# Performance work log

Hardware: AMD Instinct MI355X
Metric: run time of the kernel (lower is better)

## Reference

```python
import jax, jax.numpy as jnp
import numpy as np

B, N, DIM = 2, 2048, 1024
HEADS, DIM_HEAD = 16, 64
SCALE = DIM_HEAD ** -0.5
MASK_VALUE = -jnp.finfo(jnp.float32).max


def setup_inputs() -> dict:
    key = jax.random.key(0)
    ks = jax.random.split(key, 7)
    inner = HEADS * DIM_HEAD
    x = jax.random.normal(ks[0], (B, N, DIM), dtype=jnp.float32)
    mask = jax.random.randint(ks[1], (B, 1, N, N), 0, 2, dtype=jnp.int32)
    Wq = jax.random.normal(ks[2], (DIM, inner), dtype=jnp.float32) * (DIM ** -0.5)
    Wk = jax.random.normal(ks[3], (DIM, inner), dtype=jnp.float32) * (DIM ** -0.5)
    Wv = jax.random.normal(ks[4], (DIM, inner), dtype=jnp.float32) * (DIM ** -0.5)
    Wo = jax.random.normal(ks[5], (inner, DIM), dtype=jnp.float32) * (inner ** -0.5)
    bo = jnp.zeros((DIM,), dtype=jnp.float32)
    return {"x": x, "mask": mask, "Wq": Wq, "Wk": Wk, "Wv": Wv, "Wo": Wo, "bo": bo}


def reference(x, mask, Wq, Wk, Wv, Wo, bo):
    b, n, _ = x.shape
    # projections -> [b, h, n, d]
    def split_heads(t):
        return t.reshape(b, n, HEADS, DIM_HEAD).transpose(0, 2, 1, 3)
    q = split_heads(x @ Wq)
    k = split_heads(x @ Wk)
    v = split_heads(x @ Wv)
    # full attention scores [b, h, i, j]
    dots = jnp.einsum('bhid,bhjd->bhij', q, k) * SCALE
    # faithful to source: bin_mask = (mask == 0); fill where ~bin_mask
    bin_mask = (mask == 0)
    dots = jnp.where(bin_mask, dots, MASK_VALUE)
    attn = jax.nn.softmax(dots, axis=-1)  # dropout p=0.0 -> identity
    out = jnp.einsum('bhij,bhjd->bhid', attn, v)
    out = out.transpose(0, 2, 1, 3).reshape(b, n, HEADS * DIM_HEAD)
    return out @ Wo + bo
```

## Files before the change

### kernel.cpp

```cpp
#include <hip/hip_runtime.h>
#include <cstdint>
#include <cstddef>

typedef float    f32x4  __attribute__((ext_vector_type(4)));
typedef __bf16   bf16x8 __attribute__((ext_vector_type(8)));
typedef unsigned u32x4  __attribute__((ext_vector_type(4)));
typedef unsigned u32x2  __attribute__((ext_vector_type(2)));
typedef unsigned short u16;
typedef unsigned int   u32;

#define SCL2E 0.18033688011112042f

static __device__ __forceinline__ u16 f2bf(float f) {
    u32 u = __builtin_bit_cast(u32, f);
    u32 r = (u + 0x7FFFu + ((u >> 16) & 1u)) >> 16;
    return (u16)r;
}

static __device__ __forceinline__ u32 cvtpk_bf16(float lo, float hi) {
    u32 r;
    asm("v_cvt_pk_bf16_f32 %0, %1, %2" : "=v"(r) : "v"(lo), "v"(hi));
    return r;
}

static __device__ __forceinline__ float fexp2(float x) {
    float r;
    asm("v_exp_f32 %0, %1" : "=v"(r) : "v"(x));
    return r;
}

static __device__ __forceinline__ void gll16(const u16* g, void* l) {
    __builtin_amdgcn_global_load_lds((const __attribute__((address_space(1))) void*)g,
                                     (__attribute__((address_space(3))) void*)l, 16, 0, 0);
}


__global__ __launch_bounds__(256) void prep_k(
    const float* __restrict__ x, u16* __restrict__ xb,
    const float* __restrict__ W0, const float* __restrict__ W1,
    const float* __restrict__ W2, const float* __restrict__ W3,
    u16* __restrict__ T0, u16* __restrict__ T1,
    u16* __restrict__ T2, u16* __restrict__ T3,
    const int* __restrict__ mask, u32* __restrict__ mp)
{
    __shared__ float T[64][65];
    const int bid = blockIdx.x;
    if (bid < 2048) {
        const long i = ((long)bid * 256 + threadIdx.x) * 8;
        f32x4 a = *(const f32x4*)(x + i);
        f32x4 c = *(const f32x4*)(x + i + 4);
        u32x4 o;
        o[0] = (u32)f2bf(a[0]) | ((u32)f2bf(a[1]) << 16);
        o[1] = (u32)f2bf(a[2]) | ((u32)f2bf(a[3]) << 16);
        o[2] = (u32)f2bf(c[0]) | ((u32)f2bf(c[1]) << 16);
        o[3] = (u32)f2bf(c[2]) | ((u32)f2bf(c[3]) << 16);
        *(u32x4*)(xb + i) = o;
    } else if (bid < 3072) {
        const int idx = bid - 2048;
        const int z = idx >> 8, rem = idx & 255;
        const int n0 = (rem & 15) * 64, k0 = (rem >> 4) * 64;
        const float* W = (z == 0) ? W0 : (z == 1) ? W1 : (z == 2) ? W2 : W3;
        u16* Wt = (z == 0) ? T0 : (z == 1) ? T1 : (z == 2) ? T2 : T3;
        const float scl = (z == 0) ? SCL2E : 1.0f;
        const int c = threadIdx.x & 63, r0 = (threadIdx.x >> 6) * 16;
#pragma unroll
        for (int i = 0; i < 16; ++i)
            T[r0 + i][c] = W[(long)(k0 + r0 + i) * 1024 + n0 + c];
        __syncthreads();
#pragma unroll
        for (int i = 0; i < 16; ++i)
            Wt[(long)(n0 + r0 + i) * 1024 + k0 + c] = f2bf(T[c][r0 + i] * scl);
    } else {
        const long wi = (long)(bid - 3072) * 256 + threadIdx.x;
        const int* src = mask + wi * 32;
        u32 word = 0;
#pragma unroll
        for (int c = 0; c < 8; ++c) {
            const int4 v = *(const int4*)(src + c * 4);
            word |= (u32)(v.x != 0) << (c * 4);
            word |= (u32)(v.y != 0) << (c * 4 + 1);
            word |= (u32)(v.z != 0) << (c * 4 + 2);
            word |= (u32)(v.w != 0) << (c * 4 + 3);
        }
        mp[wi] = word;
    }
}

__global__ __launch_bounds__(256) void vt_k(const u16* __restrict__ v, u16* __restrict__ vt) {
    __shared__ u16 T[64][66];
    const int nt = blockIdx.x, h = blockIdx.y, b = blockIdx.z;
    const int c = threadIdx.x & 63, r0 = (threadIdx.x >> 6) * 16;
    const u16* src = v + ((long)b * 2048 + nt * 64) * 1024 + h * 64;
    u16* dst = vt + ((long)(b * 16 + h) * 64) * 2048 + nt * 64;
#pragma unroll
    for (int i = 0; i < 16; ++i)
        T[r0 + i][c] = src[(long)(r0 + i) * 1024 + c];
    __syncthreads();
#pragma unroll
    for (int i = 0; i < 16; ++i)
        dst[(long)(r0 + i) * 2048 + c] = T[c][r0 + i];
}


__global__ __launch_bounds__(256, 3) void gemm_qkv(
    const u16* __restrict__ A, const u16* __restrict__ Bt, u16* __restrict__ C0)
{
    constexpr int K = 1024;
    __shared__ u16 As[2][128 * 32];
    __shared__ u16 Bs[2][128 * 32];
    const int tid = threadIdx.x;
    const int wave = tid >> 6, lane = tid & 63;
    const int wr = wave >> 1, wc = wave & 1;
    const int g = lane >> 4, lr = lane & 15;
    const long mBase = (long)blockIdx.y * 128;
    const long nBase = (long)blockIdx.x * 128;

    f32x4 acc[4][4];
#pragma unroll
    for (int i = 0; i < 4; ++i)
#pragma unroll
        for (int j = 0; j < 4; ++j) acc[i][j] = f32x4{0.f, 0.f, 0.f, 0.f};

    const int o0 = tid * 16, o1 = (256 + tid) * 16;
    const int r0 = o0 >> 6, cb0 = o0 & 63;
    const int r1 = o1 >> 6, cb1 = o1 & 63;

    gll16(A  + (mBase + r0) * K + (cb0 >> 1), (char*)&As[0][0] + o0);
    gll16(A  + (mBase + r1) * K + (cb1 >> 1), (char*)&As[0][0] + o1);
    gll16(Bt + (nBase + r0) * K + (cb0 >> 1), (char*)&Bs[0][0] + o0);
    gll16(Bt + (nBase + r1) * K + (cb1 >> 1), (char*)&Bs[0][0] + o1);
    __syncthreads();

#pragma unroll 2
    for (int kt = 0; kt < 32; ++kt) {
        const int buf = kt & 1;
        if (kt + 1 < 32) {
            const long ko = (long)(kt + 1) * 32;
            gll16(A  + (mBase + r0) * K + ko + (cb0 >> 1), (char*)&As[buf ^ 1][0] + o0);
            gll16(A  + (mBase + r1) * K + ko + (cb1 >> 1), (char*)&As[buf ^ 1][0] + o1);
            gll16(Bt + (nBase + r0) * K + ko + (cb0 >> 1), (char*)&Bs[buf ^ 1][0] + o0);
            gll16(Bt + (nBase + r1) * K + ko + (cb1 >> 1), (char*)&Bs[buf ^ 1][0] + o1);
        }
        bf16x8 af[4], bfv[4];
#pragma unroll
        for (int mi = 0; mi < 4; ++mi)
            af[mi] = *(const bf16x8*)((const char*)&As[buf][0] + (wr * 64 + mi * 16 + lr) * 64 + g * 16);
#pragma unroll
        for (int ni = 0; ni < 4; ++ni)
            bfv[ni] = *(const bf16x8*)((const char*)&Bs[buf][0] + (wc * 64 + ni * 16 + lr) * 64 + g * 16);
#pragma unroll
        for (int mi = 0; mi < 4; ++mi)
#pragma unroll
            for (int ni = 0; ni < 4; ++ni)
                acc[mi][ni] = __builtin_amdgcn_mfma_f32_16x16x32_bf16(af[mi], bfv[ni], acc[mi][ni], 0, 0, 0);
        __syncthreads();
    }

    const int wsel = (int)(nBase >> 10);
    u16* Cw = C0 + (long)wsel * (4096l * 1024);
    const long ncl = nBase & 1023;
#pragma unroll
    for (int mi = 0; mi < 4; ++mi)
#pragma unroll
        for (int r = 0; r < 4; ++r) {
            const long row = mBase + wr * 64 + mi * 16 + g * 4 + r;
#pragma unroll
            for (int ni = 0; ni < 4; ++ni) {
                const long col = ncl + wc * 64 + ni * 16 + lr;
                Cw[row * 1024 + col] = f2bf(acc[mi][ni][r]);
            }
        }
}


__global__ __launch_bounds__(256, 2) void gemm_out(
    const u16* __restrict__ A, const u16* __restrict__ Bt,
    float* __restrict__ Cf, const float* __restrict__ bias)
{
    constexpr int K = 1024, N = 1024;
    __shared__ u16 As[2][64 * 32];
    __shared__ u16 Bs[2][128 * 32];
    const int tid = threadIdx.x;
    const int wave = tid >> 6, lane = tid & 63;
    const int wr = wave >> 1, wc = wave & 1;
    const int g = lane >> 4, lr = lane & 15;
    const long mBase = (long)blockIdx.y * 64;
    const long nBase = (long)blockIdx.x * 128;

    f32x4 acc[2][4];
#pragma unroll
    for (int i = 0; i < 2; ++i)
#pragma unroll
        for (int j = 0; j < 4; ++j) acc[i][j] = f32x4{0.f, 0.f, 0.f, 0.f};

    const int oA = tid * 16;
    const int rA = oA >> 6, cbA = oA & 63;
    const int o0 = tid * 16, o1 = (256 + tid) * 16;
    const int r0 = o0 >> 6, cb0 = o0 & 63;
    const int r1 = o1 >> 6, cb1 = o1 & 63;

    gll16(A  + (mBase + rA) * K + (cbA >> 1), (char*)&As[0][0] + oA);
    gll16(Bt + (nBase + r0) * K + (cb0 >> 1), (char*)&Bs[0][0] + o0);
    gll16(Bt + (nBase + r1) * K + (cb1 >> 1), (char*)&Bs[0][0] + o1);
    __syncthreads();

#pragma unroll 2
    for (int kt = 0; kt < 32; ++kt) {
        const int buf = kt & 1;
        if (kt + 1 < 32) {
            const long ko = (long)(kt + 1) * 32;
            gll16(A  + (mBase + rA) * K + ko + (cbA >> 1), (char*)&As[buf ^ 1][0] + oA);
            gll16(Bt + (nBase + r0) * K + ko + (cb0 >> 1), (char*)&Bs[buf ^ 1][0] + o0);
            gll16(Bt + (nBase + r1) * K + ko + (cb1 >> 1), (char*)&Bs[buf ^ 1][0] + o1);
        }
        bf16x8 af[2], bfv[4];
#pragma unroll
        for (int mi = 0; mi < 2; ++mi)
            af[mi] = *(const bf16x8*)((const char*)&As[buf][0] + (wr * 32 + mi * 16 + lr) * 64 + g * 16);
#pragma unroll
        for (int ni = 0; ni < 4; ++ni)
            bfv[ni] = *(const bf16x8*)((const char*)&Bs[buf][0] + (wc * 64 + ni * 16 + lr) * 64 + g * 16);
#pragma unroll
        for (int mi = 0; mi < 2; ++mi)
#pragma unroll
            for (int ni = 0; ni < 4; ++ni)
                acc[mi][ni] = __builtin_amdgcn_mfma_f32_16x16x32_bf16(af[mi], bfv[ni], acc[mi][ni], 0, 0, 0);
        __syncthreads();
    }

#pragma unroll
    for (int mi = 0; mi < 2; ++mi)
#pragma unroll
        for (int r = 0; r < 4; ++r) {
            const long row = mBase + wr * 32 + mi * 16 + g * 4 + r;
#pragma unroll
            for (int ni = 0; ni < 4; ++ni) {
                const long col = nBase + wc * 64 + ni * 16 + lr;
                Cf[row * N + col] = acc[mi][ni][r] + bias[col];
            }
        }
}


__global__ __launch_bounds__(512, 2) void attn_fwd(
    const u16* __restrict__ Qg_, const u16* __restrict__ Kg_, const u16* __restrict__ Vtg_,
    const u32* __restrict__ maskp, u16* __restrict__ Og_)
{
    __shared__ u16 Ks[2][2][64 * 64];
    __shared__ u16 Vs[2][2][64 * 64];

    const int tid = threadIdx.x, w = tid >> 6, lane = tid & 63;
    const int g = lane >> 4, lr = lane & 15;
    const int L = blockIdx.x;
    const int slot = L >> 3;
    const int grp = (L & 7) + 8 * (slot >> 3);
    const int q0 = (slot & 7) * 256;
    const int b = grp >> 4, h = grp & 15;
    const u16* Qg = Qg_ + ((long)b * 2048) * 1024 + h * 64;
    const u16* Kg = Kg_ + ((long)b * 2048) * 1024 + h * 64;
    const u16* Vtg = Vtg_ + ((long)grp * 64) * 2048;
    u16* Og = Og_ + ((long)b * 2048) * 1024 + h * 64;

    const int ldso = tid * 16;
    const int m = ldso >> 7, cb = ldso & 127;
    const int sb = cb ^ ((m & 7) << 4);
    const int kap = ((m >> 4) & 1) * 32 + ((m >> 2) & 3) * 8 + ((m >> 5) & 1) * 4 + (m & 3);
    const long ksrc = (long)kap * 1024 + (sb >> 1);
    const long vsrc = (long)m * 2048 + (sb >> 1);

    bf16x8 qf[2][2];
#pragma unroll
    for (int nq = 0; nq < 2; ++nq)
#pragma unroll
        for (int ks = 0; ks < 2; ++ks)
            qf[nq][ks] = *(const bf16x8*)(Qg + (long)(q0 + w * 32 + nq * 16 + lr) * 1024 + ks * 32 + g * 8);

    const long mrow0 = (long)b * 2048 + q0 + w * 32 + lr;
    const u32* mpr0 = maskp + mrow0 * 64;
    const u32* mpr1 = maskp + (mrow0 + 16) * 64;

    u32x4 mwC0 = *(const u32x4*)(mpr0);
    u32x4 mwC1 = *(const u32x4*)(mpr1);
#pragma unroll
    for (int hh = 0; hh < 2; ++hh) {
        gll16(Kg + hh * 65536 + ksrc, (char*)&Ks[0][hh][0] + ldso);
        gll16(Vtg + hh * 64 + vsrc, (char*)&Vs[0][hh][0] + ldso);
    }
    __syncthreads();

    const int swz = (lr & 7) << 4;
    int kb[2];
#pragma unroll
    for (int ks = 0; ks < 2; ++ks) kb[ks] = (ks * 64 + g * 16) ^ swz;

    f32x4 oacc[2][4];
#pragma unroll
    for (int i = 0; i < 2; ++i)
#pragma unroll
        for (int j = 0; j < 4; ++j) oacc[i][j] = f32x4{0.f, 0.f, 0.f, 0.f};
    f32x4 osum[2];
    osum[0] = f32x4{0.f, 0.f, 0.f, 0.f};
    osum[1] = f32x4{0.f, 0.f, 0.f, 0.f};
    const f32x4 z4 = {0.f, 0.f, 0.f, 0.f};
    const u32x4 ones4 = {0x3F803F80u, 0x3F803F80u, 0x3F803F80u, 0x3F803F80u};
    const bf16x8 ones8 = __builtin_bit_cast(bf16x8, ones4);

#pragma unroll 2
    for (int t = 0; t < 16; ++t) {
        const int cur = t & 1;
        u32x4 mwN0, mwN1;
        if (t + 1 < 16) {
            mwN0 = *(const u32x4*)(mpr0 + (t + 1) * 4);
            mwN1 = *(const u32x4*)(mpr1 + (t + 1) * 4);
            const long kv0 = (long)(t + 1) * 128;
#pragma unroll
            for (int hh = 0; hh < 2; ++hh) {
                gll16(Kg + (kv0 + hh * 64) * 1024 + ksrc, (char*)&Ks[cur ^ 1][hh][0] + ldso);
                gll16(Vtg + kv0 + hh * 64 + vsrc, (char*)&Vs[cur ^ 1][hh][0] + ldso);
            }
        }

#pragma unroll
        for (int hh = 0; hh < 2; ++hh) {
            const char* kbase = (const char*)&Ks[cur][hh][0];
            const char* vbase = (const char*)&Vs[cur][hh][0];

            f32x4 s[4][2];
            __builtin_amdgcn_s_setprio(1);
#pragma unroll
            for (int mt = 0; mt < 4; ++mt) {
                const bf16x8 kf0 = *(const bf16x8*)(kbase + (mt * 16 + lr) * 128 + kb[0]);
                const bf16x8 kf1 = *(const bf16x8*)(kbase + (mt * 16 + lr) * 128 + kb[1]);
#pragma unroll
                for (int nq = 0; nq < 2; ++nq) {
                    s[mt][nq] = __builtin_amdgcn_mfma_f32_16x16x32_bf16(kf0, qf[nq][0], z4, 0, 0, 0);
                    s[mt][nq] = __builtin_amdgcn_mfma_f32_16x16x32_bf16(kf1, qf[nq][1], s[mt][nq], 0, 0, 0);
                }
            }
            __builtin_amdgcn_s_setprio(0);

            u32 pk[4][2][2];
#pragma unroll
            for (int ts = 0; ts < 4; ++ts) {
                const int sh = g * 8 + (ts >> 1) * 4;
                const int wi = hh * 2 + (ts & 1);
#pragma unroll
                for (int nq = 0; nq < 2; ++nq) {
                    const u32 word = nq ? mwC1[wi] : mwC0[wi];
                    const u32 iwsh = (~word) >> sh;
                    float e[4];
#pragma unroll
                    for (int r = 0; r < 4; ++r) {
                        const float ev = fexp2(s[ts][nq][r]);
                        const u32 keep = (u32)__builtin_amdgcn_sbfe((int)iwsh, (u32)r, 1u);
                        e[r] = __builtin_bit_cast(float, __builtin_bit_cast(u32, ev) & keep);
                    }
                    pk[ts][nq][0] = cvtpk_bf16(e[0], e[1]);
                    pk[ts][nq][1] = cvtpk_bf16(e[2], e[3]);
                }
            }

            bf16x8 pa[2][2];
#pragma unroll
            for (int nq = 0; nq < 2; ++nq)
#pragma unroll
                for (int ks = 0; ks < 2; ++ks) {
                    u32x4 t4;
                    t4[0] = pk[ks][nq][0]; t4[1] = pk[ks][nq][1];
                    t4[2] = pk[ks + 2][nq][0]; t4[3] = pk[ks + 2][nq][1];
                    pa[nq][ks] = __builtin_bit_cast(bf16x8, t4);
                }
            __builtin_amdgcn_s_setprio(1);
#pragma unroll
            for (int nq = 0; nq < 2; ++nq)
#pragma unroll
                for (int ks = 0; ks < 2; ++ks)
                    osum[nq] = __builtin_amdgcn_mfma_f32_16x16x32_bf16(pa[nq][ks], ones8, osum[nq], 0, 0, 0);
#pragma unroll
            for (int dt = 0; dt < 4; ++dt)
#pragma unroll
                for (int ks = 0; ks < 2; ++ks) {
                    const bf16x8 vf = *(const bf16x8*)(vbase + (dt * 16 + lr) * 128 + kb[ks]);
#pragma unroll
                    for (int nq = 0; nq < 2; ++nq)
                        oacc[nq][dt] = __builtin_amdgcn_mfma_f32_16x16x32_bf16(pa[nq][ks], vf, oacc[nq][dt], 0, 0, 0);
                }
            __builtin_amdgcn_s_setprio(0);
        }
        __syncthreads();

        mwC0 = mwN0; mwC1 = mwN1;
    }

#pragma unroll
    for (int nq = 0; nq < 2; ++nq)
#pragma unroll
        for (int rr = 0; rr < 4; ++rr) {
            const float inv = __builtin_amdgcn_rcpf(osum[nq][rr]);
            const long row = (long)q0 + w * 32 + nq * 16 + g * 4 + rr;
#pragma unroll
            for (int dt = 0; dt < 4; ++dt)
                Og[row * 1024 + dt * 16 + lr] = f2bf(oacc[nq][dt][rr] * inv);
        }
}


extern "C" void kernel_launch(void* const* d_in, const int* in_sizes, int n_in,
                              void* d_out, int out_size, void* d_ws, size_t ws_size,
                              hipStream_t stream)
{
    (void)in_sizes; (void)n_in; (void)out_size; (void)ws_size;
    const float* x    = (const float*)d_in[0];
    const int*   mask = (const int*)d_in[1];
    const float* Wq   = (const float*)d_in[2];
    const float* Wk   = (const float*)d_in[3];
    const float* Wv   = (const float*)d_in[4];
    const float* Wo   = (const float*)d_in[5];
    const float* bo   = (const float*)d_in[6];
    float* out = (float*)d_out;

    char* ws = (char*)d_ws;
    u16* xb    = (u16*)(ws);
    u16* vtws  = (u16*)(ws);
    u16* WqT   = (u16*)(ws + (8l  << 20));
    u16* WkT   = (u16*)(ws + (10l << 20));
    u16* WvT   = (u16*)(ws + (12l << 20));
    u16* WoT   = (u16*)(ws + (14l << 20));
    u16* qws   = (u16*)(ws + (16l << 20));
    u16* kws   = (u16*)(ws + (24l << 20));
    u16* vws   = (u16*)(ws + (32l << 20));
    u16* inner = (u16*)(ws + (40l << 20));
    u32* mp    = (u32*)(ws + (48l << 20));

    prep_k<<<4096, 256, 0, stream>>>(x, xb, Wq, Wk, Wv, Wo, WqT, WkT, WvT, WoT, mask, mp);
    gemm_qkv<<<dim3(24, 32), 256, 0, stream>>>(xb, WqT, qws);
    vt_k<<<dim3(32, 16, 2), 256, 0, stream>>>(vws, vtws);
    attn_fwd<<<256, 512, 0, stream>>>(qws, kws, vtws, mp, inner);
    gemm_out<<<dim3(8, 64), 256, 0, stream>>>(inner, WoT, out, bo);
}
```

Measured before the change: 130.6 us.

## Rewrite QKV GEMM with 256x256 tiles, swizzled LDS and interleaved load/MFMA schedule

Replaces the 128x128-tile, 4-wave QKV projection GEMM with a 256x256-tile, 8-wave kernel that uses a 64-wide K step, an XOR-swizzled LDS layout to avoid bank conflicts, and an XCD-aware block-to-tile mapping. The K loop is split into four phases, each issuing part of the next tile's global-to-LDS loads between MFMA bursts, with s_setprio and explicit barriers and vmcnt waits. The aim is more data reuse per tile and better overlap of memory and matrix work. In exchange it needs far more LDS and registers, and the grid shrinks to 192 blocks, which fills the device less evenly.

After: 128.3 us. No clear change (-1.8%).

```diff
diff --git a/kernel.cpp b/kernel.cpp
--- a/kernel.cpp
+++ b/kernel.cpp
@@ -32,6 +32,10 @@
 static __device__ __forceinline__ void gll16(const u16* g, void* l) {
     __builtin_amdgcn_global_load_lds((const __attribute__((address_space(1))) void*)g,
                                      (__attribute__((address_space(3))) void*)l, 16, 0, 0);
+}
+
+static __device__ __forceinline__ void bar() {
+    asm volatile("s_barrier" ::: "memory");
 }
 
 
@@ -102,73 +106,155 @@
 }
 
 
-__global__ __launch_bounds__(256, 3) void gemm_qkv(
-    const u16* __restrict__ A, const u16* __restrict__ Bt, u16* __restrict__ C0)
+__global__ __launch_bounds__(512, 2) void gemm_qkv(
+    const u16* __restrict__ Ag, const u16* __restrict__ Btg, u16* __restrict__ C0)
 {
-    constexpr int K = 1024;
-    __shared__ u16 As[2][128 * 32];
-    __shared__ u16 Bs[2][128 * 32];
-    const int tid = threadIdx.x;
-    const int wave = tid >> 6, lane = tid & 63;
-    const int wr = wave >> 1, wc = wave & 1;
+    __shared__ u16 Asm[2][256 * 64];
+    __shared__ u16 Bsm[2][256 * 64];
+
+    const int tid = threadIdx.x, lane = tid & 63, w = tid >> 6;
+    const int wm = w >> 2, wn = w & 3;
     const int g = lane >> 4, lr = lane & 15;
-    const long mBase = (long)blockIdx.y * 128;
-    const long nBase = (long)blockIdx.x * 128;
-
-    f32x4 acc[4][4];
-#pragma unroll
-    for (int i = 0; i < 4; ++i)
+
+    const int L = blockIdx.x;
+    const int xcd = L & 7, idx = L >> 3;
+    const long mBase = (long)((xcd & 3) * 4 + (idx & 3)) * 256;
+    const long nBase = (long)((xcd >> 2) * 6 + (idx >> 2)) * 256;
+
+    const int srow = tid >> 3;
+    const int scolb = ((tid & 7) << 4) ^ ((srow & 7) << 4);
+    const long aoff = (mBase + srow) * 1024 + (scolb >> 1);
+    const long boff = (nBase + srow) * 1024 + (scolb >> 1);
+    const int ldst = tid * 16;
+
+    int kb[2];
+#pragma unroll
+    for (int ks = 0; ks < 2; ++ks) kb[ks] = (ks * 64 + g * 16) ^ ((lr & 7) << 4);
+
+    auto stA = [&](int d, int h, int kt) {
+        gll16(Ag + aoff + (long)h * 131072 + (long)kt * 64,
+              (char*)&Asm[d][0] + h * 16384 + ldst);
+        gll16(Ag + aoff + (long)h * 131072 + 65536 + (long)kt * 64,
+              (char*)&Asm[d][0] + h * 16384 + 8192 + ldst);
+    };
+    auto stB = [&](int d, int h, int kt) {
+        gll16(Btg + boff + (long)h * 131072 + (long)kt * 64,
+              (char*)&Bsm[d][0] + h * 16384 + ldst);
+        gll16(Btg + boff + (long)h * 131072 + 65536 + (long)kt * 64,
+              (char*)&Bsm[d][0] + h * 16384 + 8192 + ldst);
+    };
+    auto rdA = [&](int d, int mi, int ks) {
+        return *(const bf16x8*)((const char*)&Asm[d][0] + (wm * 128 + mi * 16 + lr) * 128 + kb[ks]);
+    };
+    auto rdB = [&](int d, int ni, int ks) {
+        return *(const bf16x8*)((const char*)&Bsm[d][0] + (wn * 64 + ni * 16 + lr) * 128 + kb[ks]);
+    };
+
+    f32x4 acc[8][4];
+#pragma unroll
+    for (int i = 0; i < 8; ++i)
 #pragma unroll
         for (int j = 0; j < 4; ++j) acc[i][j] = f32x4{0.f, 0.f, 0.f, 0.f};
 
-    const int o0 = tid * 16, o1 = (256 + tid) * 16;
-    const int r0 = o0 >> 6, cb0 = o0 & 63;
-    const int r1 = o1 >> 6, cb1 = o1 & 63;
-
-    gll16(A  + (mBase + r0) * K + (cb0 >> 1), (char*)&As[0][0] + o0);
-    gll16(A  + (mBase + r1) * K + (cb1 >> 1), (char*)&As[0][0] + o1);
-    gll16(Bt + (nBase + r0) * K + (cb0 >> 1), (char*)&Bs[0][0] + o0);
-    gll16(Bt + (nBase + r1) * K + (cb1 >> 1), (char*)&Bs[0][0] + o1);
-    __syncthreads();
-
-#pragma unroll 2
-    for (int kt = 0; kt < 32; ++kt) {
-        const int buf = kt & 1;
-        if (kt + 1 < 32) {
-            const long ko = (long)(kt + 1) * 32;
-            gll16(A  + (mBase + r0) * K + ko + (cb0 >> 1), (char*)&As[buf ^ 1][0] + o0);
-            gll16(A  + (mBase + r1) * K + ko + (cb1 >> 1), (char*)&As[buf ^ 1][0] + o1);
-            gll16(Bt + (nBase + r0) * K + ko + (cb0 >> 1), (char*)&Bs[buf ^ 1][0] + o0);
-            gll16(Bt + (nBase + r1) * K + ko + (cb1 >> 1), (char*)&Bs[buf ^ 1][0] + o1);
-        }
-        bf16x8 af[4], bfv[4];
+    stB(0, 0, 0); stB(0, 1, 0);
+    stA(0, 0, 0); stA(0, 1, 0);
+    stB(1, 0, 1); stB(1, 1, 1);
+    asm volatile("s_waitcnt vmcnt(4)" ::: "memory");
+    bar();
+
+    auto ktile = [&](int d, int ktA, int ktB, bool doA, bool doB, int vm) {
+        bf16x8 af[4][2], bfr[4][2];
+#pragma unroll
+        for (int mi = 0; mi < 4; ++mi) {
+            af[mi][0] = rdA(d, mi, 0);
+            af[mi][1] = rdA(d, mi, 1);
+        }
+#pragma unroll
+        for (int ni = 0; ni < 2; ++ni) {
+            bfr[ni][0] = rdB(d, ni, 0);
+            bfr[ni][1] = rdB(d, ni, 1);
+        }
+        if (doA) stA(d ^ 1, 0, ktA);
+        bar();
+        __builtin_amdgcn_s_setprio(1);
 #pragma unroll
         for (int mi = 0; mi < 4; ++mi)
-            af[mi] = *(const bf16x8*)((const char*)&As[buf][0] + (wr * 64 + mi * 16 + lr) * 64 + g * 16);
-#pragma unroll
-        for (int ni = 0; ni < 4; ++ni)
-            bfv[ni] = *(const bf16x8*)((const char*)&Bs[buf][0] + (wc * 64 + ni * 16 + lr) * 64 + g * 16);
+#pragma unroll
+            for (int ni = 0; ni < 2; ++ni) {
+                acc[mi][ni] = __builtin_amdgcn_mfma_f32_16x16x32_bf16(af[mi][0], bfr[ni][0], acc[mi][ni], 0, 0, 0);
+                acc[mi][ni] = __builtin_amdgcn_mfma_f32_16x16x32_bf16(af[mi][1], bfr[ni][1], acc[mi][ni], 0, 0, 0);
+            }
+        __builtin_amdgcn_s_setprio(0);
+        bar();
+#pragma unroll
+        for (int ni = 2; ni < 4; ++ni) {
+            bfr[ni][0] = rdB(d, ni, 0);
+            bfr[ni][1] = rdB(d, ni, 1);
+        }
+        if (doA) stA(d ^ 1, 1, ktA);
+        bar();
+        __builtin_amdgcn_s_setprio(1);
 #pragma unroll
         for (int mi = 0; mi < 4; ++mi)
 #pragma unroll
-            for (int ni = 0; ni < 4; ++ni)
-                acc[mi][ni] = __builtin_amdgcn_mfma_f32_16x16x32_bf16(af[mi], bfv[ni], acc[mi][ni], 0, 0, 0);
-        __syncthreads();
+            for (int ni = 2; ni < 4; ++ni) {
+                acc[mi][ni] = __builtin_amdgcn_mfma_f32_16x16x32_bf16(af[mi][0], bfr[ni][0], acc[mi][ni], 0, 0, 0);
+                acc[mi][ni] = __builtin_amdgcn_mfma_f32_16x16x32_bf16(af[mi][1], bfr[ni][1], acc[mi][ni], 0, 0, 0);
+            }
+        __builtin_amdgcn_s_setprio(0);
+        bar();
+#pragma unroll
+        for (int mi = 0; mi < 4; ++mi) {
+            af[mi][0] = rdA(d, mi + 4, 0);
+            af[mi][1] = rdA(d, mi + 4, 1);
+        }
+        if (doB) stB(d, 0, ktB);
+        bar();
+        __builtin_amdgcn_s_setprio(1);
+#pragma unroll
+        for (int mi = 0; mi < 4; ++mi)
+#pragma unroll
+            for (int ni = 0; ni < 2; ++ni) {
+                acc[mi + 4][ni] = __builtin_amdgcn_mfma_f32_16x16x32_bf16(af[mi][0], bfr[ni][0], acc[mi + 4][ni], 0, 0, 0);
+                acc[mi + 4][ni] = __builtin_amdgcn_mfma_f32_16x16x32_bf16(af[mi][1], bfr[ni][1], acc[mi + 4][ni], 0, 0, 0);
+            }
+        __builtin_amdgcn_s_setprio(0);
+        bar();
+        if (doB) stB(d, 1, ktB);
+        bar();
+        __builtin_amdgcn_s_setprio(1);
+#pragma unroll
+        for (int mi = 0; mi < 4; ++mi)
+#pragma unroll
+            for (int ni = 2; ni < 4; ++ni) {
+                acc[mi + 4][ni] = __builtin_amdgcn_mfma_f32_16x16x32_bf16(af[mi][0], bfr[ni][0], acc[mi + 4][ni], 0, 0, 0);
+                acc[mi + 4][ni] = __builtin_amdgcn_mfma_f32_16x16x32_bf16(af[mi][1], bfr[ni][1], acc[mi + 4][ni], 0, 0, 0);
+            }
+        __builtin_amdgcn_s_setprio(0);
+        if (vm == 0)      asm volatile("s_waitcnt vmcnt(4)" ::: "memory");
+        else if (vm == 1) asm volatile("s_waitcnt vmcnt(0)" ::: "memory");
+        bar();
+    };
+
+    for (int c = 0; c < 14; c += 2) {
+        ktile(0, c + 1, c + 2, true, true, 0);
+        ktile(1, c + 2, c + 3, true, true, 0);
     }
+    ktile(0, 15, 16, true, false, 1);
+    ktile(1, 16, 17, false, false, 2);
 
     const int wsel = (int)(nBase >> 10);
     u16* Cw = C0 + (long)wsel * (4096l * 1024);
-    const long ncl = nBase & 1023;
-#pragma unroll
-    for (int mi = 0; mi < 4; ++mi)
+    const long ncl = (nBase & 1023) + wn * 64;
+    const long rbase = mBase + wm * 128;
+#pragma unroll
+    for (int mi = 0; mi < 8; ++mi)
 #pragma unroll
         for (int r = 0; r < 4; ++r) {
-            const long row = mBase + wr * 64 + mi * 16 + g * 4 + r;
-#pragma unroll
-            for (int ni = 0; ni < 4; ++ni) {
-                const long col = ncl + wc * 64 + ni * 16 + lr;
-                Cw[row * 1024 + col] = f2bf(acc[mi][ni][r]);
-            }
+            const long row = rbase + mi * 16 + g * 4 + r;
+#pragma unroll
+            for (int ni = 0; ni < 4; ++ni)
+                Cw[row * 1024 + ncl + ni * 16 + lr] = f2bf(acc[mi][ni][r]);
         }
 }
 
@@ -433,7 +519,7 @@
     u32* mp    = (u32*)(ws + (48l << 20));
 
     prep_k<<<4096, 256, 0, stream>>>(x, xb, Wq, Wk, Wv, Wo, WqT, WkT, WvT, WoT, mask, mp);
-    gemm_qkv<<<dim3(24, 32), 256, 0, stream>>>(xb, WqT, qws);
+    gemm_qkv<<<192, 512, 0, stream>>>(xb, WqT, qws);
     vt_k<<<dim3(32, 16, 2), 256, 0, stream>>>(vws, vtws);
     attn_fwd<<<256, 512, 0, stream>>>(qws, kws, vtws, mp, inner);
     gemm_out<<<dim3(8, 64), 256, 0, stream>>>(inner, WoT, out, bo);
```
